# Kernel tuning notes

Hardware: AMD Instinct MI355X
Metric: run time of the kernel (lower is better)

The kernel has to match this reference:

```python
import jax, jax.numpy as jnp
import numpy as np

HIDDEN = 512
HEADS = 8
DHEAD = HIDDEN // HEADS  # 64


def setup_inputs() -> dict:
    key = jax.random.key(0)
    ks = jax.random.split(key, 12)
    B, S = 2, 2048
    inp = {
        "q": jax.random.normal(ks[0], (B, S, HIDDEN), dtype=jnp.float32),
        "k": jax.random.normal(ks[1], (B, S, HIDDEN), dtype=jnp.float32),
        "v": jax.random.normal(ks[2], (B, S, HIDDEN), dtype=jnp.float32),
        "mask": jnp.zeros((B, 1, 1, S), dtype=bool),
    }
    scale = 1.0 / np.sqrt(HIDDEN)
    for i, name in enumerate(["Wq", "Wk", "Wv", "Wm"]):
        inp[name] = jax.random.normal(ks[3 + i], (HIDDEN, HIDDEN), dtype=jnp.float32) * scale
    for i, name in enumerate(["bq", "bk", "bv", "bm"]):
        inp[name] = jax.random.normal(ks[7 + i], (HIDDEN,), dtype=jnp.float32) * 0.01
    return inp


def reference(q, k, v, mask, Wq, Wk, Wv, Wm, bq, bk, bv, bm):
    B = q.shape[0]
    # Linear projections (torch Linear: x @ W.T + b)
    qh = (jnp.einsum("bsd,ed->bse", q, Wq) + bq).reshape(B, HEADS, -1, DHEAD)
    kh = (jnp.einsum("bsd,ed->bse", k, Wk) + bk).reshape(B, HEADS, -1, DHEAD)
    vh = (jnp.einsum("bsd,ed->bse", v, Wv) + bv).reshape(B, HEADS, -1, DHEAD)
    # NOTE: the original module reshapes [B,S,512] -> [B,8,S',64] directly
    # (splitting the sequence dim into heads, not the hidden dim); replicated here.
    s = jnp.einsum("bhqd,bhkd->bhqk", qh, kh) / jnp.sqrt(jnp.float32(DHEAD))
    s = jnp.where(mask, jnp.float32(-1e9), s)
    s = jax.nn.softmax(s, axis=-1)
    # dropout is identity in eval mode
    attn = jnp.einsum("bhqk,bhkd->bhqd", s, vh)  # [B,H,S',64]
    attn = attn.transpose(0, 2, 1, 3).reshape(B, -1, HIDDEN)
    return jnp.einsum("bsd,ed->bse", attn, Wm) + bm
```

## Files before the change

### kernel.cpp

```cpp
#include <hip/hip_runtime.h>
#include <hip/hip_bf16.h>
#include <math.h>

typedef float  f32x4 __attribute__((ext_vector_type(4)));
typedef short  s16x8 __attribute__((ext_vector_type(8)));
typedef short  s16x4 __attribute__((ext_vector_type(4)));
typedef unsigned short u16x4 __attribute__((ext_vector_type(4)));

__device__ inline unsigned short bfc(float f){
  __hip_bfloat16 h = __float2bfloat16(f);
  unsigned short u; __builtin_memcpy(&u, &h, 2); return u;
}

__device__ inline f32x4 mfma16(s16x4 a, s16x4 b, f32x4 c){
#if __has_builtin(__builtin_amdgcn_mfma_f32_16x16x16_bf16)
  return __builtin_amdgcn_mfma_f32_16x16x16_bf16(a, b, c, 0, 0, 0);
#elif __has_builtin(__builtin_amdgcn_mfma_f32_16x16x16bf16_1k)
  return __builtin_amdgcn_mfma_f32_16x16x16bf16_1k(a, b, c, 0, 0, 0);
#else
  asm("v_mfma_f32_16x16x16_bf16 %0, %1, %2, %0" : "+v"(c) : "v"(a), "v"(b));
  return c;
#endif
}

__device__ inline void gl_lds16(const unsigned short* g, unsigned short* l){
  __builtin_amdgcn_global_load_lds(
      (const __attribute__((address_space(1))) unsigned int*)g,
      (__attribute__((address_space(3))) unsigned int*)l, 16, 0, 0);
}

__global__ __launch_bounds__(256) void prep(const float* __restrict__ q, const float* __restrict__ k,
                                            const float* __restrict__ v,
                                            const float* __restrict__ w0, const float* __restrict__ w1,
                                            const float* __restrict__ w2, const float* __restrict__ w3,
                                            const unsigned char* __restrict__ mask,
                                            unsigned short* __restrict__ AP, unsigned short* __restrict__ WP,
                                            float* __restrict__ mf){
  int y = blockIdx.y;
  int t = blockIdx.x * 256 + threadIdx.x;
  if (y < 3){
    const float* src = y==0 ? q : (y==1 ? k : v);
    unsigned short* d = AP + (size_t)y * 2097152;
    int r = t >> 6, g = t & 63;
    const float* sp = src + (size_t)r * 512 + g * 8;
    f32x4 a0 = *(const f32x4*)sp;
    f32x4 a1 = *(const f32x4*)(sp + 4);
    s16x8 o = { (short)bfc(a0.x),(short)bfc(a0.y),(short)bfc(a0.z),(short)bfc(a0.w),
                (short)bfc(a1.x),(short)bfc(a1.y),(short)bfc(a1.z),(short)bfc(a1.w) };
    size_t off = ((size_t)(((r>>4)*16 + (g>>2))*64 + (g&3)*16 + (r&15))) * 8;
    *(s16x8*)(d + off) = o;
  } else if (y < 7){
    if (blockIdx.x < 128){
      int yy = y - 3;
      const float* src = yy==0 ? w0 : yy==1 ? w1 : yy==2 ? w2 : w3;
      int c = t >> 6, g = t & 63;
      const float* sp = src + (size_t)c * 512 + g * 8;
      f32x4 a0 = *(const f32x4*)sp;
      f32x4 a1 = *(const f32x4*)(sp + 4);
      s16x8 o = { (short)bfc(a0.x),(short)bfc(a0.y),(short)bfc(a0.z),(short)bfc(a0.w),
                  (short)bfc(a1.x),(short)bfc(a1.y),(short)bfc(a1.z),(short)bfc(a1.w) };
      size_t off = ((size_t)(((c>>4)*16 + (g>>2))*64 + (g&3)*16 + (c&15))) * 8;
      *(s16x8*)(WP + yy*262144 + off) = o;
    }
  } else if (t < 4096){
    mf[t] = mask[t] ? -1.442695e9f : 0.0f;
  }
}

__global__ __launch_bounds__(256) void proj_gemm(const unsigned short* __restrict__ Ap,
    const unsigned short* __restrict__ Wp,
    const float* __restrict__ bq, const float* __restrict__ bk, const float* __restrict__ bv,
    unsigned short* __restrict__ pout, unsigned short* __restrict__ Vt){
  int z = blockIdx.z;
  const unsigned short* A = Ap + (size_t)z * 2097152;
  const unsigned short* W = Wp + (size_t)z * 262144;
  const float* bias = z==0 ? bq : (z==1 ? bk : bv);
  unsigned short* out = pout + (size_t)z * 2097152;

  int w = threadIdx.x >> 6, lane = threadIdx.x & 63;
  int lr = lane & 15, lg = lane >> 4;
  int rt = blockIdx.x * 4 + w;
  int bn = blockIdx.y;

  f32x4 acc[4] = {};
  const unsigned short* Abase = A + ((size_t)rt*8192 + lane*8);
  const unsigned short* Wbase = W + ((size_t)bn*32768 + lane*8);
#pragma unroll 4
  for (int kc = 0; kc < 16; ++kc){
    s16x8 af = *(const s16x8*)(Abase + kc*512);
#pragma unroll
    for (int n = 0; n < 4; ++n){
      s16x8 bf = *(const s16x8*)(Wbase + ((size_t)n*16 + kc)*512);
      acc[n] = __builtin_amdgcn_mfma_f32_16x16x32_bf16(af, bf, acc[n], 0, 0, 0);
    }
  }
  if (z < 2){
    int orow = rt*16 + lg*4;
#pragma unroll
    for (int n = 0; n < 4; ++n){
      int col = bn*64 + n*16 + lr;
      float bv_ = bias[col];
#pragma unroll
      for (int r = 0; r < 4; ++r)
        out[(size_t)(orow + r)*512 + col] = bfc(acc[n][r] + bv_);
    }
  } else {
    int bh = (rt >> 7) * 8 + ((rt >> 4) & 7);
    int keyb = ((rt & 15)*16 + lg*4) * 8 + bn;
    unsigned short* vt = Vt + (size_t)bh * 131072;
#pragma unroll
    for (int n = 0; n < 4; ++n){
      int col = bn*64 + n*16 + lr;
      float bv_ = bias[col];
      unsigned short* vp = vt + (size_t)(n*16 + lr) * 2048 + keyb;
#pragma unroll
      for (int r = 0; r < 4; ++r)
        vp[r*8] = bfc(acc[n][r] + bv_);
    }
  }
}

__global__ __launch_bounds__(512, 4) void flash(const unsigned short* __restrict__ Pq,
                                             const unsigned short* __restrict__ Pk,
                                             const unsigned short* __restrict__ Vt,
                                             const float* __restrict__ mf,
                                             unsigned short* __restrict__ aout){
  int qt = blockIdx.x;
  int bh = blockIdx.y;
  int b = bh >> 3, h = bh & 7;
  int w = threadIdx.x >> 6;
  int wq = w & 1, wk = w >> 1;
  int lane = threadIdx.x & 63;
  int lr = lane & 15, lg = lane >> 4;

  const unsigned short* Qh  = Pq + (size_t)(b*2048 + h*256)*512;
  const unsigned short* Kh  = Pk + (size_t)(b*2048 + h*256)*512 + (size_t)wk*32768;
  const unsigned short* Vth = Vt + (size_t)bh*131072 + wk*512;
  const float* mp = mf + b*2048 + wk*512 + lg*4;

  __shared__ char smem[65536];
  unsigned short* ktile = (unsigned short*)smem;
  unsigned short* vtile = (unsigned short*)(smem + 32768);
  float* obuf = (float*)smem;
  float* lbuf = (float*)(smem + 49152);

  int krow_l = lane >> 3;
  int cxor  = (lane & 7) ^ krow_l;
  int kcol_l = cxor * 8;

  int vhalf32 = (cxor >> 2) * 32;
  int vkc = (cxor & 3) * 8;
  const unsigned short* kg0 = Kh + (size_t)(8*(wq*2+0) + krow_l)*64 + kcol_l;
  const unsigned short* kg1 = Kh + (size_t)(8*(wq*2+1) + krow_l)*64 + kcol_l;
  const unsigned short* vg0 = Vth + (size_t)(wq*16 + 0 + krow_l + vhalf32)*2048 + vkc;
  const unsigned short* vg1 = Vth + (size_t)(wq*16 + 8 + krow_l + vhalf32)*2048 + vkc;

  s16x8 qf[2][2];
#pragma unroll
  for (int qq = 0; qq < 2; ++qq){
    int qrow = qt*64 + wq*32 + qq*16 + lr;
    qf[qq][0] = *(const s16x8*)(Qh + (size_t)qrow*64 + lg*8);
    qf[qq][1] = *(const s16x8*)(Qh + (size_t)qrow*64 + 32 + lg*8);
  }

  float l[2] = {0.f, 0.f};
  f32x4 accT[2][4] = {};
  int kswz = (lr & 7) * 16;

#define STAGE(dbuf) { \
    unsigned short* kd = ktile + ((dbuf)*4 + wk)*2048; \
    unsigned short* vd = vtile + ((dbuf)*4 + wk)*2048; \
    gl_lds16(kg0, kd + (wq*2+0)*512); \
    gl_lds16(kg1, kd + (wq*2+1)*512); \
    gl_lds16(vg0, vd + (wq*2+0)*512); \
    gl_lds16(vg1, vd + (wq*2+1)*512); \
    kg0 += 2048; kg1 += 2048; vg0 += 32; vg1 += 32; }

  STAGE(0)
  f32x4 cmv0 = *(const f32x4*)(mp);
  f32x4 cmv1 = *(const f32x4*)(mp + 16);
  mp += 32;
  __syncthreads();
  int cur = 0;

  for (int t = 0; t < 16; ++t){
    if (t < 15) STAGE(cur ^ 1)
    f32x4 nmv0, nmv1;
    if (t < 15){
      nmv0 = *(const f32x4*)(mp);
      nmv1 = *(const f32x4*)(mp + 16);
      mp += 32;
    }

    const char* kb = (const char*)(ktile + (cur*4 + wk)*2048);
    const char* vb = (const char*)(vtile + (cur*4 + wk)*2048);

    float s2[2][2][4];
    __builtin_amdgcn_s_setprio(1);
#pragma unroll
    for (int n = 0; n < 2; ++n){
      int krow = n*16 + lr;
      s16x8 kf0 = *(const s16x8*)(kb + krow*128 + ((lg*16) ^ kswz));
      s16x8 kf1 = *(const s16x8*)(kb + krow*128 + ((64 + lg*16) ^ kswz));
      f32x4 mv = n ? cmv1 : cmv0;
#pragma unroll
      for (int qq = 0; qq < 2; ++qq){
        f32x4 a = {};
        a = __builtin_amdgcn_mfma_f32_16x16x32_bf16(kf0, qf[qq][0], a, 0, 0, 0);
        a = __builtin_amdgcn_mfma_f32_16x16x32_bf16(kf1, qf[qq][1], a, 0, 0, 0);
#pragma unroll
        for (int r = 0; r < 4; ++r)
          s2[qq][n][r] = __builtin_fmaf(a[r], 0.18033688f, mv[r]);
      }
    }
    __builtin_amdgcn_s_setprio(0);

    s16x4 pf[2][2];
#pragma unroll
    for (int qq = 0; qq < 2; ++qq){
#pragma unroll
      for (int n = 0; n < 2; ++n){
        float p0 = __builtin_amdgcn_exp2f(s2[qq][n][0]);
        float p1 = __builtin_amdgcn_exp2f(s2[qq][n][1]);
        float p2 = __builtin_amdgcn_exp2f(s2[qq][n][2]);
        float p3 = __builtin_amdgcn_exp2f(s2[qq][n][3]);
        l[qq] += (p0 + p1) + (p2 + p3);
        pf[qq][n] = (s16x4){ (short)bfc(p0), (short)bfc(p1), (short)bfc(p2), (short)bfc(p3) };
      }
    }

    __builtin_amdgcn_s_setprio(1);
#pragma unroll
    for (int n = 0; n < 2; ++n){
#pragma unroll
      for (int nd = 0; nd < 4; ++nd){
        int vrow = (nd & 1)*16 + lr;
        int vchunk = ((nd >> 1)*4 + n*2 + (lg >> 1)) ^ (vrow & 7);
        s16x4 vf = *(const s16x4*)(vb + vrow*128 + vchunk*16 + (lg & 1)*8);
        accT[0][nd] = mfma16(vf, pf[0][n], accT[0][nd]);
        accT[1][nd] = mfma16(vf, pf[1][n], accT[1][nd]);
      }
    }
    __builtin_amdgcn_s_setprio(0);

    cmv0 = nmv0; cmv1 = nmv1;
    __syncthreads();
    cur ^= 1;
  }
#undef STAGE

  float lt[2];
#pragma unroll
  for (int qq = 0; qq < 2; ++qq){
    float x = l[qq] + __shfl_xor(l[qq], 16);
    lt[qq] = x + __shfl_xor(x, 32);
  }

  if (wk != 0){
    int j = wk - 1;
#pragma unroll
    for (int qq = 0; qq < 2; ++qq){
      int reg = j*4 + wq*2 + qq;
      if (lg == 0) lbuf[reg*16 + lr] = lt[qq];
#pragma unroll
      for (int nd = 0; nd < 4; ++nd)
        *(f32x4*)&obuf[((size_t)reg*64 + lane)*16 + nd*4] = accT[qq][nd];
    }
  }
  __syncthreads();
  if (wk == 0){
#pragma unroll
    for (int qq = 0; qq < 2; ++qq){
      float ltot = lt[qq];
#pragma unroll
      for (int j = 0; j < 3; ++j)
        ltot += lbuf[(j*4 + wq*2 + qq)*16 + lr];
      float inv = (ltot > 0.f) ? 1.f / ltot : 0.f;
      int q = qt*64 + wq*32 + qq*16 + lr;
      int rt = (b*2048 + q) >> 4;
#pragma unroll
      for (int nd = 0; nd < 4; ++nd){
        f32x4 o = accT[qq][nd];
#pragma unroll
        for (int j = 0; j < 3; ++j){
          int reg = j*4 + wq*2 + qq;
          f32x4 oj = *(const f32x4*)&obuf[((size_t)reg*64 + lane)*16 + nd*4];
          o += oj;
        }
        int g = h*8 + nd*2 + (lg >> 1);
        u16x4 ov = { bfc(o[0]*inv), bfc(o[1]*inv), bfc(o[2]*inv), bfc(o[3]*inv) };
        unsigned short* dp = aout + ((size_t)((rt*16 + (g>>2))*64 + (g&3)*16 + lr))*8 + (lg&1)*4;
        *(u16x4*)dp = ov;
      }
    }
  }
}

__global__ __launch_bounds__(256) void gemm_out(const unsigned short* __restrict__ Ap,
                                                const unsigned short* __restrict__ Wp,
                                                const float* __restrict__ bias,
                                                float* __restrict__ out){
  int w = threadIdx.x >> 6, lane = threadIdx.x & 63;
  int lr = lane & 15, lg = lane >> 4;
  int rt = blockIdx.x * 4 + w;
  int bn = blockIdx.y;
  f32x4 acc[4] = {};
  const unsigned short* Abase = Ap + ((size_t)rt*8192 + lane*8);
  const unsigned short* Wbase = Wp + ((size_t)bn*32768 + lane*8);
#pragma unroll 4
  for (int kc = 0; kc < 16; ++kc){
    s16x8 af = *(const s16x8*)(Abase + kc*512);
#pragma unroll
    for (int n = 0; n < 4; ++n){
      s16x8 bf = *(const s16x8*)(Wbase + ((size_t)n*16 + kc)*512);
      acc[n] = __builtin_amdgcn_mfma_f32_16x16x32_bf16(af, bf, acc[n], 0, 0, 0);
    }
  }
  int orow = rt*16 + lg*4;
#pragma unroll
  for (int n = 0; n < 4; ++n){
    int col = bn*64 + n*16 + lr;
    float bv_ = bias[col];
#pragma unroll
    for (int r = 0; r < 4; ++r)
      out[(size_t)(orow + r)*512 + col] = acc[n][r] + bv_;
  }
}

extern "C" void kernel_launch(void* const* d_in, const int* in_sizes, int n_in,
                              void* d_out, int out_size, void* d_ws, size_t ws_size,
                              hipStream_t stream) {
  const float* q  = (const float*)d_in[0];
  const float* k  = (const float*)d_in[1];
  const float* v  = (const float*)d_in[2];
  const unsigned char* mask = (const unsigned char*)d_in[3];
  const float* Wq = (const float*)d_in[4];
  const float* Wk = (const float*)d_in[5];
  const float* Wv = (const float*)d_in[6];
  const float* Wm = (const float*)d_in[7];
  const float* bq = (const float*)d_in[8];
  const float* bk = (const float*)d_in[9];
  const float* bv = (const float*)d_in[10];
  const float* bm = (const float*)d_in[11];

  unsigned short* ws = (unsigned short*)d_ws;
  unsigned short* WP   = ws;
  float*          MF   = (float*)(ws + 1048576);
  unsigned short* AP   = ws + 1056768;
  unsigned short* PQ   = ws + 7348224;
  unsigned short* VT   = ws + 13639680;
  unsigned short* AO   = ws + 15736832;

  prep<<<dim3(1024, 8), 256, 0, stream>>>(q, k, v, Wq, Wk, Wv, Wm, mask, AP, WP, MF);
  proj_gemm<<<dim3(64, 8, 3), 256, 0, stream>>>(AP, WP, bq, bk, bv, PQ, VT);
  flash<<<dim3(32, 16), 512, 0, stream>>>(PQ, PQ + 2097152, VT, MF, AO);
  gemm_out<<<dim3(64, 8), 256, 0, stream>>>(AO, WP + 3*262144, bm, (float*)d_out);
}
```

Measured before the change: 86.13 us.

## Repack K and V projection outputs into contiguous per-head chunked layouts

The projection GEMM now writes K and V directly into per-(batch,head) blocked layouts, with keys permuted so each flash tile reads contiguous chunks. The mask conversion gets the matching permutation of key indices. V stores become 8-byte vector writes instead of scattered 2-byte stores, and flash loads for K/V stream contiguous 2KB blocks per stage instead of strided rows. This is meant to cut uncoalesced stores in the GEMM epilogue and strided global reads in the attention loop, but it relies on the softmax and PV sum being invariant to key order.

Measured after the change: 72.93 us. 1.18x faster.

```diff
diff --git a/kernel.cpp b/kernel.cpp
--- a/kernel.cpp
+++ b/kernel.cpp
@@ -63,19 +63,20 @@
       *(s16x8*)(WP + yy*262144 + off) = o;
     }
   } else if (t < 4096){
-    mf[t] = mask[t] ? -1.442695e9f : 0.0f;
+    int b = t >> 11, kp = t & 2047;
+    int korig = (kp & 255) * 8 + (kp >> 8);
+    mf[t] = mask[b*2048 + korig] ? -1.442695e9f : 0.0f;
   }
 }
 
 __global__ __launch_bounds__(256) void proj_gemm(const unsigned short* __restrict__ Ap,
     const unsigned short* __restrict__ Wp,
     const float* __restrict__ bq, const float* __restrict__ bk, const float* __restrict__ bv,
-    unsigned short* __restrict__ pout, unsigned short* __restrict__ Vt){
+    unsigned short* __restrict__ pout, unsigned short* __restrict__ Vtp){
   int z = blockIdx.z;
   const unsigned short* A = Ap + (size_t)z * 2097152;
   const unsigned short* W = Wp + (size_t)z * 262144;
   const float* bias = z==0 ? bq : (z==1 ? bk : bv);
-  unsigned short* out = pout + (size_t)z * 2097152;
 
   int w = threadIdx.x >> 6, lane = threadIdx.x & 63;
   int lr = lane & 15, lg = lane >> 4;
@@ -94,7 +95,8 @@
       acc[n] = __builtin_amdgcn_mfma_f32_16x16x32_bf16(af, bf, acc[n], 0, 0, 0);
     }
   }
-  if (z < 2){
+  if (z == 0){
+    unsigned short* out = pout;
     int orow = rt*16 + lg*4;
 #pragma unroll
     for (int n = 0; n < 4; ++n){
@@ -104,25 +106,35 @@
       for (int r = 0; r < 4; ++r)
         out[(size_t)(orow + r)*512 + col] = bfc(acc[n][r] + bv_);
     }
+  } else if (z == 1){
+    int bh = (rt >> 7) * 8 + ((rt >> 4) & 7);
+    unsigned short* kp_ = pout + 2097152 + (size_t)bh*131072;
+    int kbase = (rt & 15)*16 + 256*bn;
+#pragma unroll
+    for (int n = 0; n < 4; ++n){
+      int col = bn*64 + n*16 + lr;
+      float bv_ = bias[col];
+#pragma unroll
+      for (int r = 0; r < 4; ++r)
+        kp_[(size_t)(kbase + lg*4 + r)*64 + n*16 + lr] = bfc(acc[n][r] + bv_);
+    }
   } else {
     int bh = (rt >> 7) * 8 + ((rt >> 4) & 7);
-    int keyb = ((rt & 15)*16 + lg*4) * 8 + bn;
-    unsigned short* vt = Vt + (size_t)bh * 131072;
+    unsigned short* chunk = Vtp + (size_t)bh*131072 + ((size_t)((rt & 15) + 16*bn))*1024;
 #pragma unroll
     for (int n = 0; n < 4; ++n){
       int col = bn*64 + n*16 + lr;
       float bv_ = bias[col];
-      unsigned short* vp = vt + (size_t)(n*16 + lr) * 2048 + keyb;
-#pragma unroll
-      for (int r = 0; r < 4; ++r)
-        vp[r*8] = bfc(acc[n][r] + bv_);
+      u16x4 ov = { bfc(acc[n][0] + bv_), bfc(acc[n][1] + bv_),
+                   bfc(acc[n][2] + bv_), bfc(acc[n][3] + bv_) };
+      *(u16x4*)(chunk + (n*16 + lr)*16 + lg*4) = ov;
     }
   }
 }
 
 __global__ __launch_bounds__(512, 4) void flash(const unsigned short* __restrict__ Pq,
-                                             const unsigned short* __restrict__ Pk,
-                                             const unsigned short* __restrict__ Vt,
+                                             const unsigned short* __restrict__ Kp,
+                                             const unsigned short* __restrict__ Vtp,
                                              const float* __restrict__ mf,
                                              unsigned short* __restrict__ aout){
   int qt = blockIdx.x;
@@ -134,8 +146,8 @@
   int lr = lane & 15, lg = lane >> 4;
 
   const unsigned short* Qh  = Pq + (size_t)(b*2048 + h*256)*512;
-  const unsigned short* Kh  = Pk + (size_t)(b*2048 + h*256)*512 + (size_t)wk*32768;
-  const unsigned short* Vth = Vt + (size_t)bh*131072 + wk*512;
+  const unsigned short* Kh  = Kp + (size_t)bh*131072 + (size_t)wk*32768;
+  const unsigned short* Vq  = Vtp + (size_t)bh*131072 + (size_t)wk*32768;
   const float* mp = mf + b*2048 + wk*512 + lg*4;
 
   __shared__ char smem[65536];
@@ -152,8 +164,9 @@
   int vkc = (cxor & 3) * 8;
   const unsigned short* kg0 = Kh + (size_t)(8*(wq*2+0) + krow_l)*64 + kcol_l;
   const unsigned short* kg1 = Kh + (size_t)(8*(wq*2+1) + krow_l)*64 + kcol_l;
-  const unsigned short* vg0 = Vth + (size_t)(wq*16 + 0 + krow_l + vhalf32)*2048 + vkc;
-  const unsigned short* vg1 = Vth + (size_t)(wq*16 + 8 + krow_l + vhalf32)*2048 + vkc;
+  int vd0 = wq*16 + krow_l + vhalf32;
+  const unsigned short* vg0 = Vq + (vkc>>4)*1024 + vd0*16 + (vkc & 15);
+  const unsigned short* vg1 = vg0 + 128;
 
   s16x8 qf[2][2];
 #pragma unroll
@@ -174,7 +187,7 @@
     gl_lds16(kg1, kd + (wq*2+1)*512); \
     gl_lds16(vg0, vd + (wq*2+0)*512); \
     gl_lds16(vg1, vd + (wq*2+1)*512); \
-    kg0 += 2048; kg1 += 2048; vg0 += 32; vg1 += 32; }
+    kg0 += 2048; kg1 += 2048; vg0 += 2048; vg1 += 2048; }
 
   STAGE(0)
   f32x4 cmv0 = *(const f32x4*)(mp);
```
